# Kernel optimization log

Hardware: AMD Instinct MI355X
Metric: run time of the kernel (lower is better)

The kernel has to match this reference:

```python
import jax, jax.numpy as jnp
import numpy as np

N = 100000
E = 1600000
IN_FEATS = 512
HIDDEN = 128
NUM_CLASSES = 2


def setup_inputs() -> dict:
    key = jax.random.key(0)
    k1, k2, k3, k4, k5, k6, k7 = jax.random.split(key, 7)
    inputs = jax.random.normal(k1, (N, IN_FEATS), dtype=jnp.float32)
    src = jax.random.randint(k2, (E,), 0, N, dtype=jnp.int64)
    dst = jax.random.randint(k3, (E,), 0, N, dtype=jnp.int64)
    # Glorot-style init like DGL GraphConv
    s1 = (6.0 / (IN_FEATS + HIDDEN)) ** 0.5
    s2 = (6.0 / (HIDDEN + NUM_CLASSES)) ** 0.5
    W1 = jax.random.uniform(k4, (IN_FEATS, HIDDEN), jnp.float32, -s1, s1)
    b1 = jnp.zeros((HIDDEN,), jnp.float32)
    W2 = jax.random.uniform(k5, (HIDDEN, NUM_CLASSES), jnp.float32, -s2, s2)
    b2 = jnp.zeros((NUM_CLASSES,), jnp.float32)
    return {"inputs": inputs, "W1": W1, "b1": b1, "W2": W2, "b2": b2,
            "src": src, "dst": dst}


def _graph_conv(x, W, b, src, dst, norm_src, norm_dst):
    # DGL GraphConv, norm='both': D_dst^{-1/2} A D_src^{-1/2} X W + b
    xw = x @ W                                   # [N, out] dense GEMM first (in >= out)
    m = (xw * norm_src[:, None])[src]            # gather messages [E, out]
    agg = jax.ops.segment_sum(m, dst, num_segments=N)  # scatter-add [N, out]
    return agg * norm_dst[:, None] + b


def reference(inputs, W1, b1, W2, b2, src, dst):
    ones = jnp.ones((src.shape[0],), jnp.float32)
    out_deg = jax.ops.segment_sum(ones, src, num_segments=N)
    in_deg = jax.ops.segment_sum(ones, dst, num_segments=N)
    norm_src = jax.lax.rsqrt(jnp.maximum(out_deg, 1.0))
    norm_dst = jax.lax.rsqrt(jnp.maximum(in_deg, 1.0))

    h = _graph_conv(inputs, W1, b1, src, dst, norm_src, norm_dst)
    h = jax.nn.relu(h)
    # dropout is identity at inference (training=False)
    h = _graph_conv(h, W2, b2, src, dst, norm_src, norm_dst)
    return jax.nn.softmax(h, axis=1)
```

## Files before the change

kernel.cpp:

```cpp
#include <hip/hip_runtime.h>
#include <math.h>

#define N_NODES 100000
#define N_EDGES 1600000
#define IN_F    512
#define HID     128

#define SH      8
#define NPB     256
#define BINS    ((N_NODES + NPB - 1) / NPB)
#define CBLK    256
#define EPB     ((N_EDGES + CBLK - 1) / CBLK)

typedef __attribute__((ext_vector_type(8))) _Float16 half8;
typedef __attribute__((ext_vector_type(2))) _Float16 half2v;
typedef __attribute__((ext_vector_type(4))) float float4v;

__device__ __forceinline__ unsigned int f16_to_e4m3bits(float xs) {
    _Float16 h = (_Float16)xs;
    unsigned short b = __builtin_bit_cast(unsigned short, h);
    unsigned int mag = (unsigned int)(b & 0x7fffu);
    mag = (mag + 0x3fu + ((mag >> 7) & 1u)) >> 7;
    if (mag > 0x7eu) mag = 0x7eu;
    return (((unsigned int)b >> 8) & 0x80u) | mag;
}

__global__ __launch_bounds__(256) void prep_kernel(const float* __restrict__ W1,
                                                   _Float16* __restrict__ W1S,
                                                   int* __restrict__ sdeg) {
    int i = blockIdx.x * 256 + threadIdx.x;
    if (i < IN_F * HID) {
        int k = i >> 7, c = i & 127;
        W1S[(size_t)(k >> 5) * 4096 + c * 32 + (k & 31)] = (_Float16)W1[i];
    }
    if (i < N_NODES) sdeg[i] = 0;
}

__global__ __launch_bounds__(256) void hist_kernel(const int* __restrict__ src,
                                                   const int* __restrict__ dst,
                                                   int* __restrict__ dbh,
                                                   int* __restrict__ sdeg) {
    __shared__ int hd[BINS];
    const int t = threadIdx.x, blk = blockIdx.x;
    for (int i = t; i < BINS; i += 256) hd[i] = 0;
    __syncthreads();
    const int e0 = blk * EPB, e1 = min(N_EDGES, e0 + EPB);
    for (int e = e0 + t; e < e1; e += 256) {
        atomicAdd(&hd[dst[e] >> SH], 1);
        atomicAdd(&sdeg[src[e]], 1);
    }
    __syncthreads();
    for (int i = t; i < BINS; i += 256)
        dbh[i * CBLK + blk] = hd[i];
}

__global__ __launch_bounds__(256) void binscan_kernel(int* __restrict__ dbh,
                                                      int* __restrict__ dtot) {
    __shared__ int sh[256];
    const int b = blockIdx.x, t = threadIdx.x;
    int* arr = dbh + (size_t)b * CBLK;
    int v = arr[t];
    sh[t] = v; __syncthreads();
#pragma unroll
    for (int d = 1; d < 256; d <<= 1) {
        int u = (t >= d) ? sh[t - d] : 0;
        __syncthreads();
        sh[t] += u;
        __syncthreads();
    }
    arr[t] = sh[t] - v;
    if (t == 255) dtot[b] = sh[255];
}

__global__ __launch_bounds__(512) void binbase_kernel(const int* __restrict__ dtot,
                                                      int* __restrict__ dbase,
                                                      int* __restrict__ offs) {
    __shared__ int sh[512];
    const int t = threadIdx.x;
    int v = (t < BINS) ? dtot[t] : 0;
    sh[t] = v; __syncthreads();
#pragma unroll
    for (int d = 1; d < 512; d <<= 1) {
        int u = (t >= d) ? sh[t - d] : 0;
        __syncthreads();
        sh[t] += u;
        __syncthreads();
    }
    if (t < BINS) dbase[t] = sh[t] - v;
    if (t == BINS - 1) { dbase[BINS] = sh[t]; offs[N_NODES] = sh[t]; }
}

__global__ __launch_bounds__(256) void scatter_bins_kernel(const int* __restrict__ src,
                                                           const int* __restrict__ dst,
                                                           const int* __restrict__ dbh,
                                                           const int* __restrict__ dbase,
                                                           unsigned int* __restrict__ es) {
    __shared__ int dcur[BINS];
    const int t = threadIdx.x, blk = blockIdx.x;
    for (int i = t; i < BINS; i += 256)
        dcur[i] = dbase[i] + dbh[i * CBLK + blk];
    __syncthreads();
    const int e0 = blk * EPB, e1 = min(N_EDGES, e0 + EPB);
    for (int e = e0 + t; e < e1; e += 256) {
        int d = dst[e], s = src[e];
        int p = atomicAdd(&dcur[d >> SH], 1);
        es[p] = ((unsigned int)(d & (NPB - 1)) << 24) | (unsigned int)s;
    }
}

__global__ __launch_bounds__(256) void finalize_kernel(const unsigned int* __restrict__ es,
                                                       const int* __restrict__ sdeg,
                                                       const int* __restrict__ dbase,
                                                       int* __restrict__ csr, int* __restrict__ offs,
                                                       float* __restrict__ norm_dst,
                                                       float* __restrict__ norm_src) {
    __shared__ int cnt[NPB], pos[NPB];
    const int t = threadIdx.x, b = blockIdx.x;
    const int start = dbase[b], end = dbase[b + 1];
    cnt[t] = 0; __syncthreads();
    for (int k = start + t; k < end; k += 256)
        atomicAdd(&cnt[es[k] >> 24], 1);
    __syncthreads();
    const int c = cnt[t];
    pos[t] = c; __syncthreads();
#pragma unroll
    for (int d = 1; d < 256; d <<= 1) {
        int u = (t >= d) ? pos[t - d] : 0;
        __syncthreads();
        pos[t] += u;
        __syncthreads();
    }
    const int excl = pos[t] - c;
    const int node = (b << SH) + t;
    if (node < N_NODES) {
        offs[node] = start + excl;
        norm_dst[node] = rsqrtf(fmaxf((float)c, 1.0f));
        norm_src[node] = rsqrtf(fmaxf((float)sdeg[node], 1.0f));
    }
    cnt[t] = start + excl;
    __syncthreads();
    for (int k = start + t; k < end; k += 256) {
        unsigned int v = es[k];
        int p = atomicAdd(&cnt[v >> 24], 1);
        csr[p] = (int)(v & 0x00FFFFFFu);
    }
}

#define AP 40
#define BP 40
__global__ __launch_bounds__(256) void gemm1_mfma_kernel(const float* __restrict__ X,
                                                         const _Float16* __restrict__ W1S,
                                                         const float* __restrict__ norm_src,
                                                         unsigned int* __restrict__ xw8) {
    __shared__ _Float16 As[2][64 * AP];
    __shared__ _Float16 Bs[2][128 * BP];

    const int t    = threadIdx.x;
    const int wave = t >> 6;
    const int lane = t & 63;
    const int m0   = blockIdx.x * 64;
    const int quad = lane >> 4;
    const int l16  = lane & 15;

    float4v acc[8];
#pragma unroll
    for (int c = 0; c < 8; c++) acc[c] = (float4v)0.f;

    const int srow = t >> 2;
    const int scol = (t & 3) * 8;
    const int sgrow = m0 + srow;
    const bool svalid = sgrow < N_NODES;
    const float* xbase = X + (size_t)sgrow * IN_F + scol;
    const int boff = (t >> 1) * BP + (t & 1) * 16;

    {
        float4 va[2];
        va[0] = va[1] = make_float4(0.f, 0.f, 0.f, 0.f);
        if (svalid) {
            const float4* xp = reinterpret_cast<const float4*>(xbase);
            va[0] = xp[0]; va[1] = xp[1];
        }
        half8 b0 = *reinterpret_cast<const half8*>(&W1S[t * 16]);
        half8 b1 = *reinterpret_cast<const half8*>(&W1S[t * 16 + 8]);
        half8 h;
        h[0]=(_Float16)va[0].x; h[1]=(_Float16)va[0].y; h[2]=(_Float16)va[0].z; h[3]=(_Float16)va[0].w;
        h[4]=(_Float16)va[1].x; h[5]=(_Float16)va[1].y; h[6]=(_Float16)va[1].z; h[7]=(_Float16)va[1].w;
        *reinterpret_cast<half8*>(&As[0][srow * AP + scol]) = h;
        *reinterpret_cast<half8*>(&Bs[0][boff])     = b0;
        *reinterpret_cast<half8*>(&Bs[0][boff + 8]) = b1;
    }

    int cur = 0;
    for (int it = 0; it < IN_F / 32; it++) {
        const int ktn = (it + 1) * 32;
        const bool more = ktn < IN_F;
        __syncthreads();

        float4 vb[2];
        half8 nb0, nb1;
        if (more) {
            if (svalid) {
                const float4* xp = reinterpret_cast<const float4*>(xbase + ktn);
                vb[0] = xp[0]; vb[1] = xp[1];
            } else {
                vb[0] = vb[1] = make_float4(0.f, 0.f, 0.f, 0.f);
            }
            nb0 = *reinterpret_cast<const half8*>(&W1S[(size_t)ktn * 128 + t * 16]);
            nb1 = *reinterpret_cast<const half8*>(&W1S[(size_t)ktn * 128 + t * 16 + 8]);
        }

        half8 afrag = *reinterpret_cast<const half8*>(
            &As[cur][(wave * 16 + l16) * AP + quad * 8]);
        half8 bf[8];
#pragma unroll
        for (int ct = 0; ct < 8; ct++)
            bf[ct] = *reinterpret_cast<const half8*>(
                &Bs[cur][(ct * 16 + l16) * BP + quad * 8]);
#pragma unroll
        for (int ct = 0; ct < 8; ct++)
            acc[ct] = __builtin_amdgcn_mfma_f32_16x16x32_f16(afrag, bf[ct], acc[ct], 0, 0, 0);

        if (more) {
            half8 h;
            h[0]=(_Float16)vb[0].x; h[1]=(_Float16)vb[0].y; h[2]=(_Float16)vb[0].z; h[3]=(_Float16)vb[0].w;
            h[4]=(_Float16)vb[1].x; h[5]=(_Float16)vb[1].y; h[6]=(_Float16)vb[1].z; h[7]=(_Float16)vb[1].w;
            *reinterpret_cast<half8*>(&As[cur ^ 1][srow * AP + scol]) = h;
            *reinterpret_cast<half8*>(&Bs[cur ^ 1][boff])     = nb0;
            *reinterpret_cast<half8*>(&Bs[cur ^ 1][boff + 8]) = nb1;
        }
        cur ^= 1;
    }

    const int grow = m0 + wave * 16 + quad * 4;
#pragma unroll
    for (int i = 0; i < 4; i++) {
        const int g = grow + i;
        if (g < N_NODES) {
            const float ss = norm_src[g] * 0.00390625f;
            unsigned int by[8];
#pragma unroll
            for (int ct = 0; ct < 8; ct++) {
                float xs = acc[ct][i] * ss;
                xs = fminf(fmaxf(xs, -1.75f), 1.75f);
                by[ct] = f16_to_e4m3bits(xs);
            }
            unsigned int w0 = by[0] | (by[1] << 8) | (by[2] << 16) | (by[3] << 24);
            unsigned int w1 = by[4] | (by[5] << 8) | (by[6] << 16) | (by[7] << 24);
            *reinterpret_cast<uint2*>(&xw8[(size_t)g * 32 + l16 * 2]) = make_uint2(w0, w1);
        }
    }
}

__global__ __launch_bounds__(256) void gather1_kernel(
        const int* __restrict__ csr, const int* __restrict__ offs,
        const unsigned int* __restrict__ xw8, const float* __restrict__ norm_dst,
        const float* __restrict__ norm_src, const float* __restrict__ b1,
        const float* __restrict__ W2, float* __restrict__ hw2) {
    const int gw   = (blockIdx.x * blockDim.x + threadIdx.x) >> 6;
    const int lane = threadIdx.x & 63;
    const int sub  = lane >> 4;
    const int l16  = lane & 15;
    const int n    = gw * 4 + sub;
    if (n >= N_NODES) return;
    const int off = offs[n], end = offs[n + 1];
    const uint2* xp = reinterpret_cast<const uint2*>(xw8);

    half2v accA = (half2v)0, accB = (half2v)0, accC = (half2v)0, accD = (half2v)0;

#define DECADD(u, aE, aO)                                                          \
    {                                                                              \
        unsigned int _u = (u);                                                     \
        unsigned int _e = ((_u & 0x00800080u) << 8) | ((_u & 0x007f007fu) << 7);   \
        unsigned int _s = _u >> 8;                                                 \
        unsigned int _o = ((_s & 0x00800080u) << 8) | ((_s & 0x007f007fu) << 7);   \
        aE += __builtin_bit_cast(half2v, _e);                                      \
        aO += __builtin_bit_cast(half2v, _o);                                      \
    }
#define ACC8(u2) { DECADD((u2).x, accA, accB) DECADD((u2).y, accC, accD) }

    int k = off;
    for (; k + 8 <= end; k += 8) {
        int s0 = csr[k], s1 = csr[k + 1], s2 = csr[k + 2], s3 = csr[k + 3];
        int s4 = csr[k + 4], s5 = csr[k + 5], s6 = csr[k + 6], s7 = csr[k + 7];
        uint2 u0 = xp[(size_t)s0 * 16 + l16];
        uint2 u1 = xp[(size_t)s1 * 16 + l16];
        uint2 u2 = xp[(size_t)s2 * 16 + l16];
        uint2 u3 = xp[(size_t)s3 * 16 + l16];
        uint2 u4 = xp[(size_t)s4 * 16 + l16];
        uint2 u5 = xp[(size_t)s5 * 16 + l16];
        uint2 u6 = xp[(size_t)s6 * 16 + l16];
        uint2 u7 = xp[(size_t)s7 * 16 + l16];
        ACC8(u0) ACC8(u1) ACC8(u2) ACC8(u3) ACC8(u4) ACC8(u5) ACC8(u6) ACC8(u7)
    }
    for (; k + 4 <= end; k += 4) {
        int s0 = csr[k], s1 = csr[k + 1], s2 = csr[k + 2], s3 = csr[k + 3];
        uint2 u0 = xp[(size_t)s0 * 16 + l16];
        uint2 u1 = xp[(size_t)s1 * 16 + l16];
        uint2 u2 = xp[(size_t)s2 * 16 + l16];
        uint2 u3 = xp[(size_t)s3 * 16 + l16];
        ACC8(u0) ACC8(u1) ACC8(u2) ACC8(u3)
    }
    for (; k < end; ++k) {
        uint2 u = xp[(size_t)csr[k] * 16 + l16];
        ACC8(u)
    }
#undef ACC8
#undef DECADD

    float a[8];
    a[0] = (float)accA[0]; a[2] = (float)accA[1];
    a[1] = (float)accB[0]; a[3] = (float)accB[1];
    a[4] = (float)accC[0]; a[6] = (float)accC[1];
    a[5] = (float)accD[0]; a[7] = (float)accD[1];

    const float nd = norm_dst[n] * 256.0f;
    float p0 = 0.f, p1 = 0.f;
#pragma unroll
    for (int ct = 0; ct < 8; ct++) {
        const int col = ct * 16 + l16;
        float h = fmaxf(a[ct] * nd + b1[col], 0.f);
        float2 w2v = reinterpret_cast<const float2*>(W2)[col];
        p0 += h * w2v.x;
        p1 += h * w2v.y;
    }
#pragma unroll
    for (int d = 1; d < 16; d <<= 1) {
        p0 += __shfl_xor(p0, d);
        p1 += __shfl_xor(p1, d);
    }
    if (l16 == 0) {
        float ns = norm_src[n];
        reinterpret_cast<float2*>(hw2)[n] = make_float2(p0 * ns, p1 * ns);
    }
}

__global__ void gather2_softmax_kernel(
        const int* __restrict__ csr, const int* __restrict__ offs,
        const float* __restrict__ hw2, const float* __restrict__ norm_dst,
        const float* __restrict__ b2, float* __restrict__ out) {
    const int w    = (blockIdx.x * blockDim.x + threadIdx.x) >> 6;
    const int lane = threadIdx.x & 63;
    const int sub  = lane >> 4, k0 = lane & 15;
    const int n = w * 4 + sub;
    if (n >= N_NODES) return;
    const int off = offs[n], end = offs[n + 1];

    float a0 = 0.f, a1 = 0.f;
    for (int k = off + k0; k < end; k += 16) {
        int s = csr[k];
        float2 v = reinterpret_cast<const float2*>(hw2)[s];
        a0 += v.x; a1 += v.y;
    }
#pragma unroll
    for (int d = 1; d < 16; d <<= 1) {
        a0 += __shfl_xor(a0, d);
        a1 += __shfl_xor(a1, d);
    }
    if (k0 == 0) {
        float nd = norm_dst[n];
        float z0 = a0 * nd + b2[0];
        float z1 = a1 * nd + b2[1];
        float m = fmaxf(z0, z1);
        float e0 = expf(z0 - m), e1 = expf(z1 - m);
        float inv = 1.f / (e0 + e1);
        reinterpret_cast<float2*>(out)[n] = make_float2(e0 * inv, e1 * inv);
    }
}

extern "C" void kernel_launch(void* const* d_in, const int* in_sizes, int n_in,
                              void* d_out, int out_size, void* d_ws, size_t ws_size,
                              hipStream_t stream) {
    const float* X   = (const float*)d_in[0];
    const float* W1  = (const float*)d_in[1];
    const float* b1  = (const float*)d_in[2];
    const float* W2  = (const float*)d_in[3];
    const float* b2  = (const float*)d_in[4];
    const int*   src = (const int*)d_in[5];
    const int*   dst = (const int*)d_in[6];
    float* out = (float*)d_out;

    const size_t N = N_NODES;
    char* ws = (char*)d_ws;
    auto alloc = [&](size_t bytes) -> char* {
        char* p = ws;
        ws += (bytes + 15) & ~(size_t)15;
        return p;
    };
    int*          dbh      = (int*)alloc((size_t)BINS * CBLK * 4);
    int*          dtot     = (int*)alloc(BINS * 4);
    int*          dbase    = (int*)alloc((BINS + 1) * 4);
    int*          sdeg     = (int*)alloc(N * 4);
    unsigned int* es       = (unsigned int*)alloc((size_t)N_EDGES * 4);
    int*          csr      = (int*)alloc((size_t)N_EDGES * 4);
    int*          offs     = (int*)alloc((N + 1) * 4);
    float*        norm_src = (float*)alloc(N * 4);
    float*        norm_dst = (float*)alloc(N * 4);
    float*        hw2      = (float*)alloc(N * 2 * 4);
    _Float16*     W1S      = (_Float16*)alloc((size_t)IN_F * HID * 2);
    unsigned int* xw8      = (unsigned int*)alloc(N * (size_t)HID);

    prep_kernel<<<(N_NODES + 255) / 256, 256, 0, stream>>>(W1, W1S, sdeg);
    hist_kernel<<<CBLK, 256, 0, stream>>>(src, dst, dbh, sdeg);
    binscan_kernel<<<BINS, 256, 0, stream>>>(dbh, dtot);
    binbase_kernel<<<1, 512, 0, stream>>>(dtot, dbase, offs);
    scatter_bins_kernel<<<CBLK, 256, 0, stream>>>(src, dst, dbh, dbase, es);
    finalize_kernel<<<BINS, 256, 0, stream>>>(es, sdeg, dbase,
                                              csr, offs, norm_dst, norm_src);
    gemm1_mfma_kernel<<<(N_NODES + 63) / 64, 256, 0, stream>>>(X, W1S, norm_src, xw8);
    gather1_kernel<<<(((N_NODES + 3) / 4) * 64 + 255) / 256, 256, 0, stream>>>(
        csr, offs, xw8, norm_dst, norm_src, b1, W2, hw2);
    gather2_softmax_kernel<<<(((int)N + 3) / 4 * 64 + 255) / 256, 256, 0, stream>>>(
        csr, offs, hw2, norm_dst, b2, out);
}
```

Measured before the change: 470.3 us.

## Replace binned two-pass CSR build with global-atomic degree count and direct scatter

Replaces the block-histogram, bin scan, bin scatter and per-bin finalize CSR construction with a simpler scheme: count in-degrees with global atomics, do a three-stage prefix scan over nodes, then scatter each edge's source straight into CSR using per-node atomic cursors. This removes the intermediate packed edge buffer and the second pass over it, and cuts shared-memory work. In exchange it relies on heavy random global atomics, and CSR order within a row becomes nondeterministic, which can change the floating-point summation order.

After: 631.3 us. +34.3%, slower.

```diff
diff --git a/kernel.cpp b/kernel.cpp
--- a/kernel.cpp
+++ b/kernel.cpp
@@ -6,11 +6,8 @@
 #define IN_F    512
 #define HID     128
 
-#define SH      8
-#define NPB     256
-#define BINS    ((N_NODES + NPB - 1) / NPB)
-#define CBLK    256
-#define EPB     ((N_EDGES + CBLK - 1) / CBLK)
+#define SBLK    391
+#define EBLK    1600
 
 typedef __attribute__((ext_vector_type(8))) _Float16 half8;
 typedef __attribute__((ext_vector_type(2))) _Float16 half2v;
@@ -27,39 +24,35 @@
 
 __global__ __launch_bounds__(256) void prep_kernel(const float* __restrict__ W1,
                                                    _Float16* __restrict__ W1S,
-                                                   int* __restrict__ sdeg) {
+                                                   int* __restrict__ sdeg,
+                                                   int* __restrict__ ddeg) {
     int i = blockIdx.x * 256 + threadIdx.x;
     if (i < IN_F * HID) {
         int k = i >> 7, c = i & 127;
         W1S[(size_t)(k >> 5) * 4096 + c * 32 + (k & 31)] = (_Float16)W1[i];
     }
-    if (i < N_NODES) sdeg[i] = 0;
+    if (i < N_NODES) { sdeg[i] = 0; ddeg[i] = 0; }
 }
 
 __global__ __launch_bounds__(256) void hist_kernel(const int* __restrict__ src,
                                                    const int* __restrict__ dst,
-                                                   int* __restrict__ dbh,
-                                                   int* __restrict__ sdeg) {
-    __shared__ int hd[BINS];
-    const int t = threadIdx.x, blk = blockIdx.x;
-    for (int i = t; i < BINS; i += 256) hd[i] = 0;
-    __syncthreads();
-    const int e0 = blk * EPB, e1 = min(N_EDGES, e0 + EPB);
-    for (int e = e0 + t; e < e1; e += 256) {
-        atomicAdd(&hd[dst[e] >> SH], 1);
+                                                   int* __restrict__ sdeg,
+                                                   int* __restrict__ ddeg) {
+    const int i = blockIdx.x * 256 + threadIdx.x;
+    const int stride = gridDim.x * 256;
+    for (int e = i; e < N_EDGES; e += stride) {
         atomicAdd(&sdeg[src[e]], 1);
-    }
-    __syncthreads();
-    for (int i = t; i < BINS; i += 256)
-        dbh[i * CBLK + blk] = hd[i];
-}
-
-__global__ __launch_bounds__(256) void binscan_kernel(int* __restrict__ dbh,
-                                                      int* __restrict__ dtot) {
+        atomicAdd(&ddeg[dst[e]], 1);
+    }
+}
+
+__global__ __launch_bounds__(256) void scanA_kernel(const int* __restrict__ ddeg,
+                                                    int* __restrict__ loc,
+                                                    int* __restrict__ btot) {
     __shared__ int sh[256];
     const int b = blockIdx.x, t = threadIdx.x;
-    int* arr = dbh + (size_t)b * CBLK;
-    int v = arr[t];
+    const int i = b * 256 + t;
+    int v = (i < N_NODES) ? ddeg[i] : 0;
     sh[t] = v; __syncthreads();
 #pragma unroll
     for (int d = 1; d < 256; d <<= 1) {
@@ -68,16 +61,16 @@
         sh[t] += u;
         __syncthreads();
     }
-    arr[t] = sh[t] - v;
-    if (t == 255) dtot[b] = sh[255];
-}
-
-__global__ __launch_bounds__(512) void binbase_kernel(const int* __restrict__ dtot,
-                                                      int* __restrict__ dbase,
-                                                      int* __restrict__ offs) {
+    if (i < N_NODES) loc[i] = sh[t] - v;
+    if (t == 255) btot[b] = sh[255];
+}
+
+__global__ __launch_bounds__(512) void scanB_kernel(const int* __restrict__ btot,
+                                                    int* __restrict__ bbase,
+                                                    int* __restrict__ offs) {
     __shared__ int sh[512];
     const int t = threadIdx.x;
-    int v = (t < BINS) ? dtot[t] : 0;
+    int v = (t < SBLK) ? btot[t] : 0;
     sh[t] = v; __syncthreads();
 #pragma unroll
     for (int d = 1; d < 512; d <<= 1) {
@@ -86,63 +79,38 @@
         sh[t] += u;
         __syncthreads();
     }
-    if (t < BINS) dbase[t] = sh[t] - v;
-    if (t == BINS - 1) { dbase[BINS] = sh[t]; offs[N_NODES] = sh[t]; }
-}
-
-__global__ __launch_bounds__(256) void scatter_bins_kernel(const int* __restrict__ src,
-                                                           const int* __restrict__ dst,
-                                                           const int* __restrict__ dbh,
-                                                           const int* __restrict__ dbase,
-                                                           unsigned int* __restrict__ es) {
-    __shared__ int dcur[BINS];
-    const int t = threadIdx.x, blk = blockIdx.x;
-    for (int i = t; i < BINS; i += 256)
-        dcur[i] = dbase[i] + dbh[i * CBLK + blk];
-    __syncthreads();
-    const int e0 = blk * EPB, e1 = min(N_EDGES, e0 + EPB);
-    for (int e = e0 + t; e < e1; e += 256) {
+    if (t < SBLK) bbase[t] = sh[t] - v;
+    if (t == SBLK - 1) offs[N_NODES] = sh[t];
+}
+
+__global__ __launch_bounds__(256) void scanC_kernel(const int* __restrict__ loc,
+                                                    const int* __restrict__ bbase,
+                                                    const int* __restrict__ sdeg,
+                                                    const int* __restrict__ ddeg,
+                                                    int* __restrict__ offs,
+                                                    int* __restrict__ cursor,
+                                                    float* __restrict__ norm_dst,
+                                                    float* __restrict__ norm_src) {
+    const int i = blockIdx.x * 256 + threadIdx.x;
+    if (i < N_NODES) {
+        const int off = bbase[i >> 8] + loc[i];
+        offs[i] = off;
+        cursor[i] = off;
+        norm_dst[i] = rsqrtf(fmaxf((float)ddeg[i], 1.0f));
+        norm_src[i] = rsqrtf(fmaxf((float)sdeg[i], 1.0f));
+    }
+}
+
+__global__ __launch_bounds__(256) void scatter_kernel(const int* __restrict__ src,
+                                                      const int* __restrict__ dst,
+                                                      int* __restrict__ cursor,
+                                                      int* __restrict__ csr) {
+    const int i = blockIdx.x * 256 + threadIdx.x;
+    const int stride = gridDim.x * 256;
+    for (int e = i; e < N_EDGES; e += stride) {
         int d = dst[e], s = src[e];
-        int p = atomicAdd(&dcur[d >> SH], 1);
-        es[p] = ((unsigned int)(d & (NPB - 1)) << 24) | (unsigned int)s;
-    }
-}
-
-__global__ __launch_bounds__(256) void finalize_kernel(const unsigned int* __restrict__ es,
-                                                       const int* __restrict__ sdeg,
-                                                       const int* __restrict__ dbase,
-                                                       int* __restrict__ csr, int* __restrict__ offs,
-                                                       float* __restrict__ norm_dst,
-                                                       float* __restrict__ norm_src) {
-    __shared__ int cnt[NPB], pos[NPB];
-    const int t = threadIdx.x, b = blockIdx.x;
-    const int start = dbase[b], end = dbase[b + 1];
-    cnt[t] = 0; __syncthreads();
-    for (int k = start + t; k < end; k += 256)
-        atomicAdd(&cnt[es[k] >> 24], 1);
-    __syncthreads();
-    const int c = cnt[t];
-    pos[t] = c; __syncthreads();
-#pragma unroll
-    for (int d = 1; d < 256; d <<= 1) {
-        int u = (t >= d) ? pos[t - d] : 0;
-        __syncthreads();
-        pos[t] += u;
-        __syncthreads();
-    }
-    const int excl = pos[t] - c;
-    const int node = (b << SH) + t;
-    if (node < N_NODES) {
-        offs[node] = start + excl;
-        norm_dst[node] = rsqrtf(fmaxf((float)c, 1.0f));
-        norm_src[node] = rsqrtf(fmaxf((float)sdeg[node], 1.0f));
-    }
-    cnt[t] = start + excl;
-    __syncthreads();
-    for (int k = start + t; k < end; k += 256) {
-        unsigned int v = es[k];
-        int p = atomicAdd(&cnt[v >> 24], 1);
-        csr[p] = (int)(v & 0x00FFFFFFu);
+        int p = atomicAdd(&cursor[d], 1);
+        csr[p] = s;
     }
 }
 
@@ -386,11 +354,12 @@
         ws += (bytes + 15) & ~(size_t)15;
         return p;
     };
-    int*          dbh      = (int*)alloc((size_t)BINS * CBLK * 4);
-    int*          dtot     = (int*)alloc(BINS * 4);
-    int*          dbase    = (int*)alloc((BINS + 1) * 4);
     int*          sdeg     = (int*)alloc(N * 4);
-    unsigned int* es       = (unsigned int*)alloc((size_t)N_EDGES * 4);
+    int*          ddeg     = (int*)alloc(N * 4);
+    int*          loc      = (int*)alloc(N * 4);
+    int*          btot     = (int*)alloc(SBLK * 4);
+    int*          bbase    = (int*)alloc(SBLK * 4);
+    int*          cursor   = (int*)alloc(N * 4);
     int*          csr      = (int*)alloc((size_t)N_EDGES * 4);
     int*          offs     = (int*)alloc((N + 1) * 4);
     float*        norm_src = (float*)alloc(N * 4);
@@ -399,13 +368,13 @@
     _Float16*     W1S      = (_Float16*)alloc((size_t)IN_F * HID * 2);
     unsigned int* xw8      = (unsigned int*)alloc(N * (size_t)HID);
 
-    prep_kernel<<<(N_NODES + 255) / 256, 256, 0, stream>>>(W1, W1S, sdeg);
-    hist_kernel<<<CBLK, 256, 0, stream>>>(src, dst, dbh, sdeg);
-    binscan_kernel<<<BINS, 256, 0, stream>>>(dbh, dtot);
-    binbase_kernel<<<1, 512, 0, stream>>>(dtot, dbase, offs);
-    scatter_bins_kernel<<<CBLK, 256, 0, stream>>>(src, dst, dbh, dbase, es);
-    finalize_kernel<<<BINS, 256, 0, stream>>>(es, sdeg, dbase,
-                                              csr, offs, norm_dst, norm_src);
+    prep_kernel<<<(N_NODES + 255) / 256, 256, 0, stream>>>(W1, W1S, sdeg, ddeg);
+    hist_kernel<<<EBLK, 256, 0, stream>>>(src, dst, sdeg, ddeg);
+    scanA_kernel<<<SBLK, 256, 0, stream>>>(ddeg, loc, btot);
+    scanB_kernel<<<1, 512, 0, stream>>>(btot, bbase, offs);
+    scanC_kernel<<<SBLK, 256, 0, stream>>>(loc, bbase, sdeg, ddeg,
+                                           offs, cursor, norm_dst, norm_src);
+    scatter_kernel<<<EBLK, 256, 0, stream>>>(src, dst, cursor, csr);
     gemm1_mfma_kernel<<<(N_NODES + 63) / 64, 256, 0, stream>>>(X, W1S, norm_src, xw8);
     gather1_kernel<<<(((N_NODES + 3) / 4) * 64 + 255) / 256, 256, 0, stream>>>(
         csr, offs, xw8, norm_dst, norm_src, b1, W2, hw2);
```
